# Kernel tuning notes

Measured on AMD Instinct MI355X. Metric: run time of the kernel, lower is better.

## Reference

```python
import jax, jax.numpy as jnp
import numpy as np

B, C_IN, L = 4, 128, 2048
HEADS, C_HEAD = 8, 32
HIDDEN = HEADS * C_HEAD  # 256
EPS = 1e-5


def setup_inputs() -> dict:
    key = jax.random.key(0)
    ks = jax.random.split(key, 6)
    return {
        "x": jax.random.normal(ks[0], (B, C_IN, L), dtype=jnp.float32),
        "w_qkv": jax.random.normal(ks[1], (3 * HIDDEN, C_IN), dtype=jnp.float32) * 0.05,
        "b_qkv": jax.random.normal(ks[2], (3 * HIDDEN,), dtype=jnp.float32) * 0.05,
        "w_out": jax.random.normal(ks[3], (C_IN, HIDDEN), dtype=jnp.float32) * 0.05,
        "b_out": jax.random.normal(ks[4], (C_IN,), dtype=jnp.float32) * 0.05,
        "bn_weight": jnp.ones((C_IN,), dtype=jnp.float32),
        "bn_bias": jnp.zeros((C_IN,), dtype=jnp.float32),
        "bn_mean": jnp.zeros((C_IN,), dtype=jnp.float32),
        "bn_var": jnp.ones((C_IN,), dtype=jnp.float32),
    }


def reference(x, w_qkv, b_qkv, w_out, b_out, bn_weight, bn_bias, bn_mean, bn_var):
    # 1x1 conv == channel matmul: (B, 3*hidden, L)
    qkv = jnp.einsum('oi,bil->bol', w_qkv, x) + b_qkv[None, :, None]
    # '(qkv heads c) l -> qkv heads l c' (batched)
    qkv = qkv.reshape(B, 3, HEADS, C_HEAD, L).transpose(1, 0, 2, 4, 3)  # (3,B,H,L,c)
    q, k, v = qkv[0], qkv[1], qkv[2]
    # Faithful quirk: original scales q by sqrt(q.shape[1]) == sqrt(L), not sqrt(c)
    q = q / jnp.sqrt(jnp.float32(L))
    # scores (B,H,L,L), softmax over last axis
    scores = jnp.einsum('bhqd,bhkd->bhqk', q, k)
    ctx = jax.nn.softmax(scores, axis=-1)
    # Faithful quirk: 'hca,hcb->hab' contracts over the QUERY axis of ctx
    attn = jnp.einsum('bhqa,bhqd->bhad', ctx, v)  # (B,H,L,c)
    # 'heads l h -> (heads h) l'
    attn = attn.transpose(0, 1, 3, 2).reshape(B, HIDDEN, L)
    out = jnp.einsum('oi,bil->bol', w_out, attn) + b_out[None, :, None]
    out = out + x
    # BatchNorm inference mode with running stats, per-channel
    inv = bn_weight / jnp.sqrt(bn_var + EPS)
    out = out * inv[None, :, None] + (bn_bias - bn_mean * inv)[None, :, None]
    return out
```

## Files before the change

kernel.cpp:

```cpp
#include <hip/hip_runtime.h>
#include <math.h>

#define BB 4
#define CIN 128
#define LL 2048
#define HH 8
#define CH 32
#define HID 256

typedef __attribute__((ext_vector_type(8))) __bf16 bf16x8;
typedef __attribute__((ext_vector_type(4))) float f32x4;
typedef __attribute__((ext_vector_type(16))) float f32x16;

static __device__ __forceinline__ unsigned int f2bf(float f) {
    union { __bf16 b; unsigned short s; } u;
    u.b = (__bf16)f;
    return (unsigned int)u.s;
}
static __device__ __forceinline__ float bf2f(unsigned int s) {
    union { float f; unsigned int u; } x;
    x.u = s << 16;
    return x.f;
}

#define MFMA   __builtin_amdgcn_mfma_f32_16x16x32_bf16
#define MFMA32 __builtin_amdgcn_mfma_f32_32x32x16_bf16
#define E2(x)  __builtin_amdgcn_exp2f(x)

__global__ __launch_bounds__(256) void prep_kernel(
        const float* __restrict__ x, const float* __restrict__ w,
        const float* __restrict__ wo,
        unsigned short* __restrict__ xb, unsigned short* __restrict__ wb,
        unsigned short* __restrict__ wob) {
    __shared__ float tr2[128][65];
    const int t = threadIdx.x;
    const int bid = blockIdx.x;
    if (bid >= 224) {
        const int idx = ((bid - 224) * 256 + t) * 4;
        float4 v = *(const float4*)(wo + idx);
        uint2 o;
        o.x = f2bf(v.x) | (f2bf(v.y) << 16);
        o.y = f2bf(v.z) | (f2bf(v.w) << 16);
        *(uint2*)(wob + idx) = o;
        return;
    }
    if (bid >= 128) {
        const int idx = ((bid - 128) * 256 + t) * 4;
        float4 v = *(const float4*)(w + idx);
        uint2 o;
        o.x = f2bf(v.x) | (f2bf(v.y) << 16);
        o.y = f2bf(v.z) | (f2bf(v.w) << 16);
        *(uint2*)(wb + idx) = o;
        return;
    }
    const int lt = bid & 31, b = bid >> 5;
    const int l0 = lt * 64;
    const int ll = t & 63, ig = t >> 6;
    const float* xp = x + (size_t)b * CIN * LL + l0 + ll;
    #pragma unroll
    for (int k = 0; k < 32; ++k) {
        const int i = k * 4 + ig;
        tr2[i][ll] = xp[(size_t)i * LL];
    }
    __syncthreads();
    const int l = t >> 2, i0 = (t & 3) * 32;
    unsigned short* dst = xb + ((size_t)b * LL + l0 + l) * CIN + i0;
    unsigned int wv[16];
    #pragma unroll
    for (int j = 0; j < 16; ++j)
        wv[j] = f2bf(tr2[i0 + 2*j][l]) | (f2bf(tr2[i0 + 2*j + 1][l]) << 16);
    *(uint4*)(dst)      = make_uint4(wv[0],  wv[1],  wv[2],  wv[3]);
    *(uint4*)(dst + 8)  = make_uint4(wv[4],  wv[5],  wv[6],  wv[7]);
    *(uint4*)(dst + 16) = make_uint4(wv[8],  wv[9],  wv[10], wv[11]);
    *(uint4*)(dst + 24) = make_uint4(wv[12], wv[13], wv[14], wv[15]);
}

__global__ __launch_bounds__(256) void qkv_mfma(
        const unsigned short* __restrict__ xb, const unsigned short* __restrict__ wb,
        const float* __restrict__ b_qkv,
        unsigned short* __restrict__ qb, unsigned short* __restrict__ kb,
        unsigned short* __restrict__ vtb) {
    __shared__ unsigned short xlds[64][136];
    __shared__ unsigned short wlds2[32][136];
    __shared__ float tr[32 * 65];
    const int t = threadIdx.x, w = t >> 6, lane = t & 63;
    const int r = lane & 15, gq = lane >> 4;
    const int lt = blockIdx.x;
    const int g  = blockIdx.y;
    const int b  = blockIdx.z;
    const int sel = g >> 3, h = g & 7;
    const int obase = sel * 256 + h * 32;
    const int l0 = lt * 64;

    {
        const unsigned short* xsrc = xb + ((size_t)b * LL + l0) * CIN;
        #pragma unroll
        for (int k2 = 0; k2 < 4; ++k2) {
            int idx = t + k2 * 256;
            int row = idx >> 4, col8 = (idx & 15) * 8;
            *(uint4*)&xlds[row][col8] = *(const uint4*)(xsrc + row * CIN + col8);
        }
        const unsigned short* wsrc = wb + (size_t)obase * CIN;
        #pragma unroll
        for (int k2 = 0; k2 < 2; ++k2) {
            int idx = t + k2 * 256;
            int row = idx >> 4, col8 = (idx & 15) * 8;
            *(uint4*)&wlds2[row][col8] = *(const uint4*)(wsrc + row * CIN + col8);
        }
    }
    __syncthreads();

    f32x4 acc0 = {0,0,0,0}, acc1 = {0,0,0,0};
    #pragma unroll
    for (int ks = 0; ks < 4; ++ks) {
        bf16x8 bfr = *(const bf16x8*)&xlds[w * 16 + r][gq * 8 + ks * 32];
        bf16x8 a0  = *(const bf16x8*)&wlds2[r][gq * 8 + ks * 32];
        bf16x8 a1  = *(const bf16x8*)&wlds2[16 + r][gq * 8 + ks * 32];
        acc0 = MFMA(a0, bfr, acc0, 0, 0, 0);
        acc1 = MFMA(a1, bfr, acc1, 0, 0, 0);
    }
    const float scale = (sel == 0) ? 0.03187935835f : 1.0f;
    #pragma unroll
    for (int reg = 0; reg < 4; ++reg) {
        const int oc0 = gq * 4 + reg;
        tr[oc0 * 65 + w * 16 + r] = (acc0[reg] + b_qkv[obase + oc0]) * scale;
        const int oc1 = 16 + gq * 4 + reg;
        tr[oc1 * 65 + w * 16 + r] = (acc1[reg] + b_qkv[obase + oc1]) * scale;
    }
    __syncthreads();

    if (sel == 2) {
        unsigned short* dst = vtb + ((size_t)(b * HH + h) * CH) * LL + l0;
        #pragma unroll
        for (int rr = 0; rr < 8; ++rr) {
            int flat = rr * 256 + t;
            int c = flat >> 6, l = flat & 63;
            dst[(size_t)c * LL + l] = (unsigned short)f2bf(tr[c * 65 + l]);
        }
    } else {
        unsigned short* dst = (sel == 0 ? qb : kb)
                              + ((size_t)(b * HH + h) * LL + l0) * CH;
        #pragma unroll
        for (int rr = 0; rr < 8; ++rr) {
            int flat = rr * 256 + t;
            int c = flat & 31, lr = flat >> 5;
            dst[flat] = (unsigned short)f2bf(tr[c * 65 + lr]);
        }
    }
}

__global__ __launch_bounds__(512, 4) void denom_mfma(
        const unsigned short* __restrict__ qb,
        const unsigned short* __restrict__ kb,
        unsigned short* __restrict__ vtb) {
    __shared__ unsigned short klds[2][128][40];
    __shared__ float zz[128];
    const int t = threadIdx.x, wave = t >> 6, lane = t & 63;
    const int id = blockIdx.x;
    const int bh = (id & 7) * 4 + (id >> 7);
    const int qt = (id >> 3) & 15;
    const int r = lane & 15, g = lane >> 4;
    const int q0 = qt * 128 + wave * 16;

    bf16x8 afrag = *(const bf16x8*)(qb + ((size_t)bh * LL + q0 + r) * CH + 8 * g);

    const unsigned short* ksrc = kb + ((size_t)bh * LL + (t >> 2)) * CH + (t & 3) * 8;
    const int sdst = (t >> 2) * 40 + (t & 3) * 8;

    float z0 = 0.f, z1 = 0.f, z2 = 0.f, z3 = 0.f;
    const f32x4 zero = {0.f, 0.f, 0.f, 0.f};

    *(uint4*)(&klds[0][0][0] + sdst) = *(const uint4*)(ksrc);
    __syncthreads();

    const int rb = r * 40 + 8 * g;
    for (int c = 0; c < 16; ++c) {
        const int cur = c & 1;
        uint4 nreg;
        if (c < 15)
            nreg = *(const uint4*)(ksrc + (size_t)(c + 1) * 4096);
        const unsigned short* kc = &klds[cur][0][0];
        #pragma unroll
        for (int s = 0; s < 8; ++s) {
            bf16x8 bf = *(const bf16x8*)(kc + s * 16 * 40 + rb);
            f32x4 d = MFMA(afrag, bf, zero, 0, 0, 0);
            z0 += E2(d[0]); z1 += E2(d[1]); z2 += E2(d[2]); z3 += E2(d[3]);
        }
        if (c < 15)
            *(uint4*)(&klds[cur ^ 1][0][0] + sdst) = nreg;
        __syncthreads();
    }

    #pragma unroll
    for (int m = 1; m < 16; m <<= 1) {
        z0 += __shfl_xor(z0, m); z1 += __shfl_xor(z1, m);
        z2 += __shfl_xor(z2, m); z3 += __shfl_xor(z3, m);
    }
    if (r == 0)
        *(float4*)&zz[wave * 16 + 4 * g] = make_float4(z0, z1, z2, z3);
    __syncthreads();
    if (t < 128) zz[t] = 1.0f / zz[t];
    __syncthreads();

    const int d = t >> 4, qo = (t & 15) * 8;
    unsigned short* vrow = vtb + ((size_t)bh * CH + d) * LL + qt * 128 + qo;
    uint4 v = *(const uint4*)vrow;
    const float* zp = &zz[qo];
    unsigned int w0, w1, w2, w3;
    w0 = f2bf(bf2f(v.x & 0xFFFFu) * zp[0]) | (f2bf(bf2f(v.x >> 16) * zp[1]) << 16);
    w1 = f2bf(bf2f(v.y & 0xFFFFu) * zp[2]) | (f2bf(bf2f(v.y >> 16) * zp[3]) << 16);
    w2 = f2bf(bf2f(v.z & 0xFFFFu) * zp[4]) | (f2bf(bf2f(v.z >> 16) * zp[5]) << 16);
    w3 = f2bf(bf2f(v.w & 0xFFFFu) * zp[6]) | (f2bf(bf2f(v.w >> 16) * zp[7]) << 16);
    *(uint4*)vrow = make_uint4(w0, w1, w2, w3);
}

__global__ __launch_bounds__(512, 4) void attn_mfma(
        const unsigned short* __restrict__ qb,
        const unsigned short* __restrict__ kb,
        const unsigned short* __restrict__ vtb,
        float* __restrict__ attnT) {
    __shared__ unsigned short qlds[2][64][40];
    __shared__ unsigned short vlds[2][64][40];
    const int t = threadIdx.x, wave = t >> 6, lane = t & 63;
    const int ln = lane & 31, hi = lane >> 5;
    const int id = blockIdx.x;
    const int bhqh = (id & 7) * 8 + (id >> 6);
    const int at = (id >> 3) & 7;
    const int bh = bhqh >> 1, qh = bhqh & 1;
    const int b = bh >> 3, h = bh & 7;
    const int a0 = at * 256 + wave * 32;
    const int q00 = qh * 1024;

    const unsigned short* kp = kb + ((size_t)bh * LL + a0 + ln) * CH + 8 * hi;
    const bf16x8 kf0 = *(const bf16x8*)kp;
    const bf16x8 kf1 = *(const bf16x8*)(kp + 16);

    const int ts = t & 255;
    const unsigned short* qsrc = qb + ((size_t)bh * LL + q00 + (ts >> 2)) * CH
                                 + (ts & 3) * 8;
    const int vsub = ts >> 7, vd = (ts >> 2) & 31, vq = (ts & 3) * 8;
    const unsigned short* vsrc = vtb + ((size_t)bh * CH + vd) * LL + q00
                                 + vsub * 32 + vq;
    const int sdstq = (ts >> 2) * 40 + (ts & 3) * 8;
    const int sdstv = (vsub * 32 + vd) * 40 + vq;
    unsigned short* const ql0 = &qlds[0][0][0];
    unsigned short* const ql1 = &qlds[1][0][0];
    unsigned short* const vl0 = &vlds[0][0][0];
    unsigned short* const vl1 = &vlds[1][0][0];

    f32x16 acc = {0.f,0.f,0.f,0.f,0.f,0.f,0.f,0.f,0.f,0.f,0.f,0.f,0.f,0.f,0.f,0.f};
    const f32x16 zero16 = {0.f,0.f,0.f,0.f,0.f,0.f,0.f,0.f,0.f,0.f,0.f,0.f,0.f,0.f,0.f,0.f};

#define CVTPK(dst, lo_, hi_) \
    asm("v_cvt_pk_bf16_f32 %0, %1, %2" : "=v"(dst) : "v"(lo_), "v"(hi_))
#define SWAPH(a_, b_) \
    asm("v_permlane32_swap_b32 %0, %1" : "+v"(a_), "+v"(b_))

    if (wave < 4) *(uint4*)(ql0 + sdstq) = *(const uint4*)(qsrc);
    else          *(uint4*)(vl0 + sdstv) = *(const uint4*)(vsrc);
    __syncthreads();

    for (int n = 0; n < 16; ++n) {
        const int cur = n & 1;
        uint4 nreg;
        if (n < 15) {
            if (wave < 4) nreg = *(const uint4*)(qsrc + (size_t)(n + 1) * 2048);
            else          nreg = *(const uint4*)(vsrc + (n + 1) * 64);
        }
        const unsigned short* qc = cur ? ql1 : ql0;
        const unsigned short* vc = cur ? vl1 : vl0;
        #pragma unroll
        for (int s2 = 0; s2 < 2; ++s2) {
            const int rdq = (s2 * 32 + ln) * 40 + 8 * hi;
            bf16x8 qa0 = *(const bf16x8*)(qc + rdq);
            bf16x8 qa1 = *(const bf16x8*)(qc + rdq + 16);
            bf16x8 vb0 = *(const bf16x8*)(vc + rdq);
            bf16x8 vb1 = *(const bf16x8*)(vc + rdq + 16);
            f32x16 s = MFMA32(qa0, kf0, zero16, 0, 0, 0);
            s = MFMA32(qa1, kf1, s, 0, 0, 0);
            unsigned int w0, w1, w2, w3, w4, w5, w6, w7;
            {
                float p0  = E2(s[0]),  p1  = E2(s[1]),  p2  = E2(s[2]),  p3  = E2(s[3]);
                float p4  = E2(s[4]),  p5  = E2(s[5]),  p6  = E2(s[6]),  p7  = E2(s[7]);
                float p8  = E2(s[8]),  p9  = E2(s[9]),  p10 = E2(s[10]), p11 = E2(s[11]);
                float p12 = E2(s[12]), p13 = E2(s[13]), p14 = E2(s[14]), p15 = E2(s[15]);
                CVTPK(w0, p0,  p1);  CVTPK(w1, p2,  p3);
                CVTPK(w2, p4,  p5);  CVTPK(w3, p6,  p7);
                CVTPK(w4, p8,  p9);  CVTPK(w5, p10, p11);
                CVTPK(w6, p12, p13); CVTPK(w7, p14, p15);
                SWAPH(w0, w2); SWAPH(w1, w3); SWAPH(w4, w6); SWAPH(w5, w7);
            }
            union { uint4 u; bf16x8 v; } pa0, pa1;
            pa0.u = make_uint4(w0, w1, w2, w3);
            pa1.u = make_uint4(w4, w5, w6, w7);
            __builtin_amdgcn_s_setprio(1);
            acc = MFMA32(pa0.v, vb0, acc, 0, 0, 0);
            acc = MFMA32(pa1.v, vb1, acc, 0, 0, 0);
            __builtin_amdgcn_s_setprio(0);
        }
        if (n < 15) {
            if (wave < 4) *(uint4*)((cur ? ql0 : ql1) + sdstq) = nreg;
            else          *(uint4*)((cur ? vl0 : vl1) + sdstv) = nreg;
        }
        __syncthreads();
    }

#undef SWAPH
#undef CVTPK

    float* ob = attnT + ((size_t)qh * BB * HID + (size_t)b * HID + h * CH + ln) * LL
                + a0 + 4 * hi;
    *(f32x4*)(ob +  0) = __builtin_shufflevector(acc, acc,  0,  1,  2,  3);
    *(f32x4*)(ob +  8) = __builtin_shufflevector(acc, acc,  4,  5,  6,  7);
    *(f32x4*)(ob + 16) = __builtin_shufflevector(acc, acc,  8,  9, 10, 11);
    *(f32x4*)(ob + 24) = __builtin_shufflevector(acc, acc, 12, 13, 14, 15);
}

__global__ __launch_bounds__(256, 4) void out_mfma(
        const float* __restrict__ attnT, const unsigned short* __restrict__ wob,
        const float* __restrict__ x, const float* __restrict__ b_out,
        const float* __restrict__ bnw, const float* __restrict__ bnb,
        const float* __restrict__ bnm, const float* __restrict__ bnv,
        float* __restrict__ out) {
    __shared__ unsigned short alds[2][32][40];
    __shared__ unsigned short wlds[2][128][40];
    const int t = threadIdx.x, wave = t >> 6, lane = t & 63;
    const int ln = lane & 31, hi = lane >> 5;
    const int id = blockIdx.x;
    const int bid = (id & 7) * 32 + (id >> 3);
    const int b = bid >> 6, lt = bid & 63;
    const int l0 = lt * 32;
    const size_t PART = (size_t)BB * HID * LL;
    const int WBUF = 128 * 40;

    const int si = t >> 3, sl4 = (t & 7) * 4;
    const float* ap0 = attnT + ((size_t)b * HID + si) * LL + l0 + sl4;
    const unsigned short* wsrc0 = wob + (size_t)(t >> 2) * HID + (t & 3) * 8;
    const unsigned short* wsrc1 = wsrc0 + (size_t)64 * HID;
    unsigned short* const wdst0 = &wlds[0][t >> 2][(t & 3) * 8];

    f32x16 acc = {0.f,0.f,0.f,0.f,0.f,0.f,0.f,0.f,0.f,0.f,0.f,0.f,0.f,0.f,0.f,0.f};

    {
        f32x4 a0 = *(const f32x4*)(ap0);
        f32x4 a1 = *(const f32x4*)(ap0 + PART);
        uint4 w0 = *(const uint4*)(wsrc0);
        uint4 w1 = *(const uint4*)(wsrc1);
        #pragma unroll
        for (int j = 0; j < 4; ++j)
            alds[0][sl4 + j][si] = (unsigned short)f2bf(a0[j] + a1[j]);
        *(uint4*)(wdst0) = w0;
        *(uint4*)(wdst0 + 64 * 40) = w1;
    }
    __syncthreads();

    for (int c = 0; c < 8; ++c) {
        const int cur = c & 1;
        f32x4 na0, na1; uint4 nw0, nw1;
        if (c < 7) {
            na0 = *(const f32x4*)(ap0 + (size_t)(c + 1) * 32 * LL);
            na1 = *(const f32x4*)(ap0 + (size_t)(c + 1) * 32 * LL + PART);
            nw0 = *(const uint4*)(wsrc0 + (c + 1) * 32);
            nw1 = *(const uint4*)(wsrc1 + (c + 1) * 32);
        }
        const unsigned short* wc = &wlds[cur][0][0] + (wave * 32 + ln) * 40 + 8 * hi;
        const unsigned short* ac = &alds[cur][0][0] + ln * 40 + 8 * hi;
        bf16x8 af0 = *(const bf16x8*)(wc);
        bf16x8 af1 = *(const bf16x8*)(wc + 16);
        bf16x8 bf0 = *(const bf16x8*)(ac);
        bf16x8 bf1 = *(const bf16x8*)(ac + 16);
        acc = MFMA32(af0, bf0, acc, 0, 0, 0);
        acc = MFMA32(af1, bf1, acc, 0, 0, 0);
        if (c < 7) {
            const int nb = cur ^ 1;
            #pragma unroll
            for (int j = 0; j < 4; ++j)
                alds[nb][sl4 + j][si] = (unsigned short)f2bf(na0[j] + na1[j]);
            *(uint4*)(wdst0 + nb * WBUF) = nw0;
            *(uint4*)(wdst0 + nb * WBUF + 64 * 40) = nw1;
        }
        __syncthreads();
    }

    #pragma unroll
    for (int reg = 0; reg < 16; ++reg) {
        const int o = wave * 32 + (reg & 3) + 8 * (reg >> 2) + 4 * hi;
        const float inv = bnw[o] / sqrtf(bnv[o] + 1e-5f);
        const float sh  = bnb[o] - bnm[o] * inv;
        const size_t idx = ((size_t)b * CIN + o) * LL + l0 + ln;
        float val = acc[reg] + b_out[o] + x[idx];
        out[idx] = val * inv + sh;
    }
}

extern "C" void kernel_launch(void* const* d_in, const int* in_sizes, int n_in,
                              void* d_out, int out_size, void* d_ws, size_t ws_size,
                              hipStream_t stream) {
    const float* x      = (const float*)d_in[0];
    const float* w_qkv  = (const float*)d_in[1];
    const float* b_qkv  = (const float*)d_in[2];
    const float* w_out  = (const float*)d_in[3];
    const float* b_out  = (const float*)d_in[4];
    const float* bnw    = (const float*)d_in[5];
    const float* bnb    = (const float*)d_in[6];
    const float* bnm    = (const float*)d_in[7];
    const float* bnv    = (const float*)d_in[8];
    float* out = (float*)d_out;

    const size_t NBH = (size_t)BB * HH;
    const size_t QKV_ELEMS = NBH * LL * CH;
    unsigned short* qb    = (unsigned short*)d_ws;
    unsigned short* kb    = qb + QKV_ELEMS;
    unsigned short* vtb   = kb + QKV_ELEMS;
    float* attnT = (float*)(vtb + QKV_ELEMS);
    unsigned short* xb  = (unsigned short*)(attnT + 2 * (size_t)BB * HID * LL);
    unsigned short* wb  = xb + (size_t)BB * LL * CIN;
    unsigned short* wob = wb + (size_t)3 * HID * CIN;

    prep_kernel<<<dim3(256), 256, 0, stream>>>(x, w_qkv, w_out, xb, wb, wob);
    qkv_mfma<<<dim3(32, 24, BB), 256, 0, stream>>>(xb, wb, b_qkv, qb, kb, vtb);
    denom_mfma<<<dim3(512), 512, 0, stream>>>(qb, kb, vtb);
    attn_mfma<<<dim3(512), 512, 0, stream>>>(qb, kb, vtb, attnT);
    out_mfma<<<dim3(256), 256, 0, stream>>>(attnT, wob, x, b_out,
                                            bnw, bnb, bnm, bnv, out);
}
```

Measured before the change: 71.18 us.

## Fuse bf16 conversion into QKV/out kernels and double tile sizes in attention

After: 70.33 us. No clear change (-1.2%).

```diff
diff --git a/kernel.cpp b/kernel.cpp
--- a/kernel.cpp
+++ b/kernel.cpp
@@ -27,124 +27,98 @@
 #define MFMA32 __builtin_amdgcn_mfma_f32_32x32x16_bf16
 #define E2(x)  __builtin_amdgcn_exp2f(x)
 
-__global__ __launch_bounds__(256) void prep_kernel(
-        const float* __restrict__ x, const float* __restrict__ w,
-        const float* __restrict__ wo,
-        unsigned short* __restrict__ xb, unsigned short* __restrict__ wb,
-        unsigned short* __restrict__ wob) {
-    __shared__ float tr2[128][65];
-    const int t = threadIdx.x;
-    const int bid = blockIdx.x;
-    if (bid >= 224) {
-        const int idx = ((bid - 224) * 256 + t) * 4;
-        float4 v = *(const float4*)(wo + idx);
-        uint2 o;
-        o.x = f2bf(v.x) | (f2bf(v.y) << 16);
-        o.y = f2bf(v.z) | (f2bf(v.w) << 16);
-        *(uint2*)(wob + idx) = o;
-        return;
-    }
-    if (bid >= 128) {
-        const int idx = ((bid - 128) * 256 + t) * 4;
-        float4 v = *(const float4*)(w + idx);
-        uint2 o;
-        o.x = f2bf(v.x) | (f2bf(v.y) << 16);
-        o.y = f2bf(v.z) | (f2bf(v.w) << 16);
-        *(uint2*)(wb + idx) = o;
-        return;
-    }
-    const int lt = bid & 31, b = bid >> 5;
-    const int l0 = lt * 64;
-    const int ll = t & 63, ig = t >> 6;
-    const float* xp = x + (size_t)b * CIN * LL + l0 + ll;
-    #pragma unroll
-    for (int k = 0; k < 32; ++k) {
-        const int i = k * 4 + ig;
-        tr2[i][ll] = xp[(size_t)i * LL];
-    }
-    __syncthreads();
-    const int l = t >> 2, i0 = (t & 3) * 32;
-    unsigned short* dst = xb + ((size_t)b * LL + l0 + l) * CIN + i0;
-    unsigned int wv[16];
-    #pragma unroll
-    for (int j = 0; j < 16; ++j)
-        wv[j] = f2bf(tr2[i0 + 2*j][l]) | (f2bf(tr2[i0 + 2*j + 1][l]) << 16);
-    *(uint4*)(dst)      = make_uint4(wv[0],  wv[1],  wv[2],  wv[3]);
-    *(uint4*)(dst + 8)  = make_uint4(wv[4],  wv[5],  wv[6],  wv[7]);
-    *(uint4*)(dst + 16) = make_uint4(wv[8],  wv[9],  wv[10], wv[11]);
-    *(uint4*)(dst + 24) = make_uint4(wv[12], wv[13], wv[14], wv[15]);
-}
-
 __global__ __launch_bounds__(256) void qkv_mfma(
-        const unsigned short* __restrict__ xb, const unsigned short* __restrict__ wb,
+        const float* __restrict__ x, const float* __restrict__ w_qkv,
         const float* __restrict__ b_qkv,
         unsigned short* __restrict__ qb, unsigned short* __restrict__ kb,
         unsigned short* __restrict__ vtb) {
-    __shared__ unsigned short xlds[64][136];
+    __shared__ float tr2[128][66];
     __shared__ unsigned short wlds2[32][136];
     __shared__ float tr[32 * 65];
     const int t = threadIdx.x, w = t >> 6, lane = t & 63;
     const int r = lane & 15, gq = lane >> 4;
     const int lt = blockIdx.x;
-    const int g  = blockIdx.y;
+    const int h  = blockIdx.y;
     const int b  = blockIdx.z;
-    const int sel = g >> 3, h = g & 7;
-    const int obase = sel * 256 + h * 32;
     const int l0 = lt * 64;
 
     {
-        const unsigned short* xsrc = xb + ((size_t)b * LL + l0) * CIN;
-        #pragma unroll
-        for (int k2 = 0; k2 < 4; ++k2) {
-            int idx = t + k2 * 256;
-            int row = idx >> 4, col8 = (idx & 15) * 8;
-            *(uint4*)&xlds[row][col8] = *(const uint4*)(xsrc + row * CIN + col8);
-        }
-        const unsigned short* wsrc = wb + (size_t)obase * CIN;
+        const int ll = t & 63, ig = t >> 6;
+        const float* xp = x + (size_t)b * CIN * LL + l0 + ll;
+        #pragma unroll
+        for (int k = 0; k < 32; ++k) {
+            const int i = k * 4 + ig;
+            tr2[i][ll] = xp[(size_t)i * LL];
+        }
+    }
+    __syncthreads();
+
+    bf16x8 bfr[4];
+    #pragma unroll
+    for (int ks = 0; ks < 4; ++ks) {
+        union { uint4 u; bf16x8 v; } p;
+        const int i0 = gq * 8 + ks * 32, lx = w * 16 + r;
+        p.u.x = f2bf(tr2[i0 + 0][lx]) | (f2bf(tr2[i0 + 1][lx]) << 16);
+        p.u.y = f2bf(tr2[i0 + 2][lx]) | (f2bf(tr2[i0 + 3][lx]) << 16);
+        p.u.z = f2bf(tr2[i0 + 4][lx]) | (f2bf(tr2[i0 + 5][lx]) << 16);
+        p.u.w = f2bf(tr2[i0 + 6][lx]) | (f2bf(tr2[i0 + 7][lx]) << 16);
+        bfr[ks] = p.v;
+    }
+
+    for (int sel = 0; sel < 3; ++sel) {
+        const int obase = sel * 256 + h * 32;
+        __syncthreads();
         #pragma unroll
         for (int k2 = 0; k2 < 2; ++k2) {
             int idx = t + k2 * 256;
             int row = idx >> 4, col8 = (idx & 15) * 8;
-            *(uint4*)&wlds2[row][col8] = *(const uint4*)(wsrc + row * CIN + col8);
-        }
-    }
-    __syncthreads();
-
-    f32x4 acc0 = {0,0,0,0}, acc1 = {0,0,0,0};
-    #pragma unroll
-    for (int ks = 0; ks < 4; ++ks) {
-        bf16x8 bfr = *(const bf16x8*)&xlds[w * 16 + r][gq * 8 + ks * 32];
-        bf16x8 a0  = *(const bf16x8*)&wlds2[r][gq * 8 + ks * 32];
-        bf16x8 a1  = *(const bf16x8*)&wlds2[16 + r][gq * 8 + ks * 32];
-        acc0 = MFMA(a0, bfr, acc0, 0, 0, 0);
-        acc1 = MFMA(a1, bfr, acc1, 0, 0, 0);
-    }
-    const float scale = (sel == 0) ? 0.03187935835f : 1.0f;
-    #pragma unroll
-    for (int reg = 0; reg < 4; ++reg) {
-        const int oc0 = gq * 4 + reg;
-        tr[oc0 * 65 + w * 16 + r] = (acc0[reg] + b_qkv[obase + oc0]) * scale;
-        const int oc1 = 16 + gq * 4 + reg;
-        tr[oc1 * 65 + w * 16 + r] = (acc1[reg] + b_qkv[obase + oc1]) * scale;
-    }
-    __syncthreads();
-
-    if (sel == 2) {
-        unsigned short* dst = vtb + ((size_t)(b * HH + h) * CH) * LL + l0;
-        #pragma unroll
-        for (int rr = 0; rr < 8; ++rr) {
-            int flat = rr * 256 + t;
-            int c = flat >> 6, l = flat & 63;
-            dst[(size_t)c * LL + l] = (unsigned short)f2bf(tr[c * 65 + l]);
-        }
-    } else {
-        unsigned short* dst = (sel == 0 ? qb : kb)
-                              + ((size_t)(b * HH + h) * LL + l0) * CH;
-        #pragma unroll
-        for (int rr = 0; rr < 8; ++rr) {
-            int flat = rr * 256 + t;
-            int c = flat & 31, lr = flat >> 5;
-            dst[flat] = (unsigned short)f2bf(tr[c * 65 + lr]);
+            const float* wsrc = w_qkv + (size_t)(obase + row) * CIN + col8;
+            float4 a4 = *(const float4*)(wsrc);
+            float4 b4 = *(const float4*)(wsrc + 4);
+            uint4 o;
+            o.x = f2bf(a4.x) | (f2bf(a4.y) << 16);
+            o.y = f2bf(a4.z) | (f2bf(a4.w) << 16);
+            o.z = f2bf(b4.x) | (f2bf(b4.y) << 16);
+            o.w = f2bf(b4.z) | (f2bf(b4.w) << 16);
+            *(uint4*)&wlds2[row][col8] = o;
+        }
+        __syncthreads();
+
+        f32x4 acc0 = {0,0,0,0}, acc1 = {0,0,0,0};
+        #pragma unroll
+        for (int ks = 0; ks < 4; ++ks) {
+            bf16x8 a0 = *(const bf16x8*)&wlds2[r][gq * 8 + ks * 32];
+            bf16x8 a1 = *(const bf16x8*)&wlds2[16 + r][gq * 8 + ks * 32];
+            acc0 = MFMA(a0, bfr[ks], acc0, 0, 0, 0);
+            acc1 = MFMA(a1, bfr[ks], acc1, 0, 0, 0);
+        }
+        const float scale = (sel == 0) ? 0.03187935835f : 1.0f;
+        #pragma unroll
+        for (int reg = 0; reg < 4; ++reg) {
+            const int oc0 = gq * 4 + reg;
+            tr[oc0 * 65 + w * 16 + r] = (acc0[reg] + b_qkv[obase + oc0]) * scale;
+            const int oc1 = 16 + gq * 4 + reg;
+            tr[oc1 * 65 + w * 16 + r] = (acc1[reg] + b_qkv[obase + oc1]) * scale;
+        }
+        __syncthreads();
+
+        if (sel == 2) {
+            unsigned short* dst = vtb + ((size_t)(b * HH + h) * CH) * LL + l0;
+            #pragma unroll
+            for (int rr = 0; rr < 8; ++rr) {
+                int flat = rr * 256 + t;
+                int c = flat >> 6, l = flat & 63;
+                dst[(size_t)c * LL + l] = (unsigned short)f2bf(tr[c * 65 + l]);
+            }
+        } else {
+            unsigned short* dst = (sel == 0 ? qb : kb)
+                                  + ((size_t)(b * HH + h) * LL + l0) * CH;
+            #pragma unroll
+            for (int rr = 0; rr < 8; ++rr) {
+                int flat = rr * 256 + t;
+                int c = flat & 31, lr = flat >> 5;
+                dst[flat] = (unsigned short)f2bf(tr[c * 65 + lr]);
+            }
         }
     }
 }
@@ -153,7 +127,7 @@
         const unsigned short* __restrict__ qb,
         const unsigned short* __restrict__ kb,
         unsigned short* __restrict__ vtb) {
-    __shared__ unsigned short klds[2][128][40];
+    __shared__ unsigned short klds[2][256][40];
     __shared__ float zz[128];
     const int t = threadIdx.x, wave = t >> 6, lane = t & 63;
     const int id = blockIdx.x;
@@ -164,30 +138,44 @@
 
     bf16x8 afrag = *(const bf16x8*)(qb + ((size_t)bh * LL + q0 + r) * CH + 8 * g);
 
-    const unsigned short* ksrc = kb + ((size_t)bh * LL + (t >> 2)) * CH + (t & 3) * 8;
-    const int sdst = (t >> 2) * 40 + (t & 3) * 8;
+    const unsigned short* kbase = kb + (size_t)bh * LL * CH;
 
     float z0 = 0.f, z1 = 0.f, z2 = 0.f, z3 = 0.f;
     const f32x4 zero = {0.f, 0.f, 0.f, 0.f};
 
-    *(uint4*)(&klds[0][0][0] + sdst) = *(const uint4*)(ksrc);
+    #pragma unroll
+    for (int k2 = 0; k2 < 2; ++k2) {
+        int ts2 = t + 512 * k2;
+        int a = ts2 >> 2, dcol = (ts2 & 3) * 8;
+        *(uint4*)(&klds[0][0][0] + a * 40 + dcol) =
+            *(const uint4*)(kbase + (size_t)a * CH + dcol);
+    }
     __syncthreads();
 
     const int rb = r * 40 + 8 * g;
-    for (int c = 0; c < 16; ++c) {
+    for (int c = 0; c < 8; ++c) {
         const int cur = c & 1;
-        uint4 nreg;
-        if (c < 15)
-            nreg = *(const uint4*)(ksrc + (size_t)(c + 1) * 4096);
+        uint4 nreg0, nreg1;
+        if (c < 7) {
+            int ts0 = t, ts1 = t + 512;
+            nreg0 = *(const uint4*)(kbase + (size_t)((c + 1) * 256 + (ts0 >> 2)) * CH
+                                    + (ts0 & 3) * 8);
+            nreg1 = *(const uint4*)(kbase + (size_t)((c + 1) * 256 + (ts1 >> 2)) * CH
+                                    + (ts1 & 3) * 8);
+        }
         const unsigned short* kc = &klds[cur][0][0];
         #pragma unroll
-        for (int s = 0; s < 8; ++s) {
+        for (int s = 0; s < 16; ++s) {
             bf16x8 bf = *(const bf16x8*)(kc + s * 16 * 40 + rb);
             f32x4 d = MFMA(afrag, bf, zero, 0, 0, 0);
             z0 += E2(d[0]); z1 += E2(d[1]); z2 += E2(d[2]); z3 += E2(d[3]);
         }
-        if (c < 15)
-            *(uint4*)(&klds[cur ^ 1][0][0] + sdst) = nreg;
+        if (c < 7) {
+            unsigned short* kd = &klds[cur ^ 1][0][0];
+            int ts0 = t, ts1 = t + 512;
+            *(uint4*)(kd + (ts0 >> 2) * 40 + (ts0 & 3) * 8) = nreg0;
+            *(uint4*)(kd + (ts1 >> 2) * 40 + (ts1 & 3) * 8) = nreg1;
+        }
         __syncthreads();
     }
 
@@ -219,8 +207,8 @@
         const unsigned short* __restrict__ kb,
         const unsigned short* __restrict__ vtb,
         float* __restrict__ attnT) {
-    __shared__ unsigned short qlds[2][64][40];
-    __shared__ unsigned short vlds[2][64][40];
+    __shared__ unsigned short qlds[2][128][40];
+    __shared__ unsigned short vlds[2][128][40];
     const int t = threadIdx.x, wave = t >> 6, lane = t & 63;
     const int ln = lane & 31, hi = lane >> 5;
     const int id = blockIdx.x;
@@ -235,19 +223,25 @@
     const bf16x8 kf0 = *(const bf16x8*)kp;
     const bf16x8 kf1 = *(const bf16x8*)(kp + 16);
 
-    const int ts = t & 255;
-    const unsigned short* qsrc = qb + ((size_t)bh * LL + q00 + (ts >> 2)) * CH
-                                 + (ts & 3) * 8;
-    const int vsub = ts >> 7, vd = (ts >> 2) & 31, vq = (ts & 3) * 8;
-    const unsigned short* vsrc = vtb + ((size_t)bh * CH + vd) * LL + q00
-                                 + vsub * 32 + vq;
-    const int sdstq = (ts >> 2) * 40 + (ts & 3) * 8;
-    const int sdstv = (vsub * 32 + vd) * 40 + vq;
     unsigned short* const ql0 = &qlds[0][0][0];
     unsigned short* const ql1 = &qlds[1][0][0];
     unsigned short* const vl0 = &vlds[0][0][0];
     unsigned short* const vl1 = &vlds[1][0][0];
 
+    const int ts = t & 255;
+    int sq[2], sv[2];
+    const unsigned short *qsa[2], *vsa[2];
+    #pragma unroll
+    for (int k2 = 0; k2 < 2; ++k2) {
+        int ts2 = ts + 256 * k2;
+        int q = ts2 >> 2, dcol = (ts2 & 3) * 8;
+        qsa[k2] = qb + ((size_t)bh * LL + q00 + q) * CH + dcol;
+        sq[k2] = q * 40 + dcol;
+        int sub = ts2 >> 7, vd = (ts2 >> 2) & 31, vq = (ts2 & 3) * 8;
+        vsa[k2] = vtb + ((size_t)bh * CH + vd) * LL + q00 + sub * 32 + vq;
+        sv[k2] = (sub * 32 + vd) * 40 + vq;
+    }
+
     f32x16 acc = {0.f,0.f,0.f,0.f,0.f,0.f,0.f,0.f,0.f,0.f,0.f,0.f,0.f,0.f,0.f,0.f};
     const f32x16 zero16 = {0.f,0.f,0.f,0.f,0.f,0.f,0.f,0.f,0.f,0.f,0.f,0.f,0.f,0.f,0.f,0.f};
 
@@ -256,21 +250,29 @@
 #define SWAPH(a_, b_) \
     asm("v_permlane32_swap_b32 %0, %1" : "+v"(a_), "+v"(b_))
 
-    if (wave < 4) *(uint4*)(ql0 + sdstq) = *(const uint4*)(qsrc);
-    else          *(uint4*)(vl0 + sdstv) = *(const uint4*)(vsrc);
-    __syncthreads();
-
-    for (int n = 0; n < 16; ++n) {
+    #pragma unroll
+    for (int k2 = 0; k2 < 2; ++k2) {
+        if (wave < 4) *(uint4*)(ql0 + sq[k2]) = *(const uint4*)(qsa[k2]);
+        else          *(uint4*)(vl0 + sv[k2]) = *(const uint4*)(vsa[k2]);
+    }
+    __syncthreads();
+
+    for (int n = 0; n < 8; ++n) {
         const int cur = n & 1;
-        uint4 nreg;
-        if (n < 15) {
-            if (wave < 4) nreg = *(const uint4*)(qsrc + (size_t)(n + 1) * 2048);
-            else          nreg = *(const uint4*)(vsrc + (n + 1) * 64);
+        uint4 nreg0, nreg1;
+        if (n < 7) {
+            if (wave < 4) {
+                nreg0 = *(const uint4*)(qsa[0] + (size_t)(n + 1) * 128 * CH);
+                nreg1 = *(const uint4*)(qsa[1] + (size_t)(n + 1) * 128 * CH);
+            } else {
+                nreg0 = *(const uint4*)(vsa[0] + (n + 1) * 128);
+                nreg1 = *(const uint4*)(vsa[1] + (n + 1) * 128);
+            }
         }
         const unsigned short* qc = cur ? ql1 : ql0;
         const unsigned short* vc = cur ? vl1 : vl0;
         #pragma unroll
-        for (int s2 = 0; s2 < 2; ++s2) {
+        for (int s2 = 0; s2 < 4; ++s2) {
             const int rdq = (s2 * 32 + ln) * 40 + 8 * hi;
             bf16x8 qa0 = *(const bf16x8*)(qc + rdq);
             bf16x8 qa1 = *(const bf16x8*)(qc + rdq + 16);
@@ -298,9 +300,16 @@
             acc = MFMA32(pa1.v, vb1, acc, 0, 0, 0);
             __builtin_amdgcn_s_setprio(0);
         }
-        if (n < 15) {
-            if (wave < 4) *(uint4*)((cur ? ql0 : ql1) + sdstq) = nreg;
-            else          *(uint4*)((cur ? vl0 : vl1) + sdstv) = nreg;
+        if (n < 7) {
+            unsigned short* qd = cur ? ql0 : ql1;
+            unsigned short* vd = cur ? vl0 : vl1;
+            if (wave < 4) {
+                *(uint4*)(qd + sq[0]) = nreg0;
+                *(uint4*)(qd + sq[1]) = nreg1;
+            } else {
+                *(uint4*)(vd + sv[0]) = nreg0;
+                *(uint4*)(vd + sv[1]) = nreg1;
+            }
         }
         __syncthreads();
     }
@@ -317,7 +326,7 @@
 }
 
 __global__ __launch_bounds__(256, 4) void out_mfma(
-        const float* __restrict__ attnT, const unsigned short* __restrict__ wob,
+        const float* __restrict__ attnT, const float* __restrict__ w_out,
         const float* __restrict__ x, const float* __restrict__ b_out,
         const float* __restrict__ bnw, const float* __restrict__ bnb,
         const float* __restrict__ bnm, const float* __restrict__ bnv,
@@ -335,33 +344,40 @@
 
     const int si = t >> 3, sl4 = (t & 7) * 4;
     const float* ap0 = attnT + ((size_t)b * HID + si) * LL + l0 + sl4;
-    const unsigned short* wsrc0 = wob + (size_t)(t >> 2) * HID + (t & 3) * 8;
-    const unsigned short* wsrc1 = wsrc0 + (size_t)64 * HID;
+    const float* wsrc0 = w_out + (size_t)(t >> 2) * HID + (t & 3) * 8;
+    const float* wsrc1 = wsrc0 + (size_t)64 * HID;
     unsigned short* const wdst0 = &wlds[0][t >> 2][(t & 3) * 8];
 
     f32x16 acc = {0.f,0.f,0.f,0.f,0.f,0.f,0.f,0.f,0.f,0.f,0.f,0.f,0.f,0.f,0.f,0.f};
+
+#define PACKW(dst, p) do { \
+    float4 a4 = *(const float4*)(p); \
+    float4 b4 = *(const float4*)((p) + 4); \
+    uint4 o_; \
+    o_.x = f2bf(a4.x) | (f2bf(a4.y) << 16); \
+    o_.y = f2bf(a4.z) | (f2bf(a4.w) << 16); \
+    o_.z = f2bf(b4.x) | (f2bf(b4.y) << 16); \
+    o_.w = f2bf(b4.z) | (f2bf(b4.w) << 16); \
+    *(uint4*)(dst) = o_; \
+} while (0)
 
     {
         f32x4 a0 = *(const f32x4*)(ap0);
         f32x4 a1 = *(const f32x4*)(ap0 + PART);
-        uint4 w0 = *(const uint4*)(wsrc0);
-        uint4 w1 = *(const uint4*)(wsrc1);
         #pragma unroll
         for (int j = 0; j < 4; ++j)
             alds[0][sl4 + j][si] = (unsigned short)f2bf(a0[j] + a1[j]);
-        *(uint4*)(wdst0) = w0;
-        *(uint4*)(wdst0 + 64 * 40) = w1;
+        PACKW(wdst0, wsrc0);
+        PACKW(wdst0 + 64 * 40, wsrc1);
     }
     __syncthreads();
 
     for (int c = 0; c < 8; ++c) {
         const int cur = c & 1;
-        f32x4 na0, na1; uint4 nw0, nw1;
+        f32x4 na0, na1;
         if (c < 7) {
             na0 = *(const f32x4*)(ap0 + (size_t)(c + 1) * 32 * LL);
             na1 = *(const f32x4*)(ap0 + (size_t)(c + 1) * 32 * LL + PART);
-            nw0 = *(const uint4*)(wsrc0 + (c + 1) * 32);
-            nw1 = *(const uint4*)(wsrc1 + (c + 1) * 32);
         }
         const unsigned short* wc = &wlds[cur][0][0] + (wave * 32 + ln) * 40 + 8 * hi;
         const unsigned short* ac = &alds[cur][0][0] + ln * 40 + 8 * hi;
@@ -376,11 +392,12 @@
             #pragma unroll
             for (int j = 0; j < 4; ++j)
                 alds[nb][sl4 + j][si] = (unsigned short)f2bf(na0[j] + na1[j]);
-            *(uint4*)(wdst0 + nb * WBUF) = nw0;
-            *(uint4*)(wdst0 + nb * WBUF + 64 * 40) = nw1;
-        }
-        __syncthreads();
-    }
+            PACKW(wdst0 + nb * WBUF, wsrc0 + (c + 1) * 32);
+            PACKW(wdst0 + nb * WBUF + 64 * 40, wsrc1 + (c + 1) * 32);
+        }
+        __syncthreads();
+    }
+#undef PACKW
 
     #pragma unroll
     for (int reg = 0; reg < 16; ++reg) {
@@ -413,14 +430,10 @@
     unsigned short* kb    = qb + QKV_ELEMS;
     unsigned short* vtb   = kb + QKV_ELEMS;
     float* attnT = (float*)(vtb + QKV_ELEMS);
-    unsigned short* xb  = (unsigned short*)(attnT + 2 * (size_t)BB * HID * LL);
-    unsigned short* wb  = xb + (size_t)BB * LL * CIN;
-    unsigned short* wob = wb + (size_t)3 * HID * CIN;
-
-    prep_kernel<<<dim3(256), 256, 0, stream>>>(x, w_qkv, w_out, xb, wb, wob);
-    qkv_mfma<<<dim3(32, 24, BB), 256, 0, stream>>>(xb, wb, b_qkv, qb, kb, vtb);
+
+    qkv_mfma<<<dim3(32, 8, BB), 256, 0, stream>>>(x, w_qkv, b_qkv, qb, kb, vtb);
     denom_mfma<<<dim3(512), 512, 0, stream>>>(qb, kb, vtb);
     attn_mfma<<<dim3(512), 512, 0, stream>>>(qb, kb, vtb, attnT);
-    out_mfma<<<dim3(256), 256, 0, stream>>>(attnT, wob, x, b_out,
+    out_mfma<<<dim3(256), 256, 0, stream>>>(attnT, w_out, x, b_out,
                                             bnw, bnb, bnm, bnv, out);
 }
```
